# Kernel tuning notes

Measured on AMD Instinct MI355X. Metric: run time of the kernel, lower is better.

## Reference

```python
import jax, jax.numpy as jnp
import numpy as np

B, H, W, C = 4, 256, 256, 128
HEADS, WS, SHIFT = 4, 8, 4
EPS = 1e-5


def _rel_pos_index(ws):
    coords = np.stack(np.meshgrid(np.arange(ws), np.arange(ws), indexing='ij'))
    cf = coords.reshape(2, -1)
    rel = (cf[:, :, None] - cf[:, None, :]).transpose(1, 2, 0)
    rel[:, :, 0] += ws - 1
    rel[:, :, 1] += ws - 1
    rel[:, :, 0] *= 2 * ws - 1
    return rel.sum(-1).reshape(-1)

REL_IDX = jnp.array(_rel_pos_index(WS))


def _shift_mask(h, w, ws, shift):
    img = np.zeros((1, h, w, 1))
    cnt = 0
    sl = (slice(0, -ws), slice(-ws, -shift), slice(-shift, None))
    for hs in sl:
        for wsl in sl:
            img[:, hs, wsl, :] = cnt
            cnt += 1
    m = img.reshape(1, h // ws, ws, w // ws, ws, 1).transpose(0, 1, 3, 2, 4, 5).reshape(-1, ws * ws)
    am = m[:, None, :] - m[:, :, None]
    return jnp.array(np.where(am != 0, -100.0, 0.0).astype(np.float32))

ATTN_MASK = _shift_mask(H, W, WS, SHIFT)  # (nW, ws*ws, ws*ws)


def _ln(x, scale, bias):
    mu = x.mean(-1, keepdims=True)
    var = x.var(-1, keepdims=True)
    return (x - mu) / jnp.sqrt(var + EPS) * scale + bias


def setup_inputs() -> dict:
    key = jax.random.key(0)
    ks = jax.random.split(key, 8)
    s = 0.02
    return dict(
        hidden_states=jax.random.normal(ks[0], (B, H * W, C), jnp.float32),
        ln1_scale=jnp.ones((C,), jnp.float32), ln1_bias=jnp.zeros((C,), jnp.float32),
        q_w=jax.random.normal(ks[1], (C, C), jnp.float32) * s, q_b=jnp.zeros((C,), jnp.float32),
        k_w=jax.random.normal(ks[2], (C, C), jnp.float32) * s, k_b=jnp.zeros((C,), jnp.float32),
        v_w=jax.random.normal(ks[3], (C, C), jnp.float32) * s, v_b=jnp.zeros((C,), jnp.float32),
        proj_w=jax.random.normal(ks[4], (C, C), jnp.float32) * s, proj_b=jnp.zeros((C,), jnp.float32),
        rpb_table=jax.random.normal(ks[5], ((2 * WS - 1) ** 2, HEADS), jnp.float32) * s,
        ln2_scale=jnp.ones((C,), jnp.float32), ln2_bias=jnp.zeros((C,), jnp.float32),
        fc1_w=jax.random.normal(ks[6], (C, 4 * C), jnp.float32) * s, fc1_b=jnp.zeros((4 * C,), jnp.float32),
        fc2_w=jax.random.normal(ks[7], (4 * C, C), jnp.float32) * s, fc2_b=jnp.zeros((C,), jnp.float32),
    )


def reference(hidden_states, ln1_scale, ln1_bias, q_w, q_b, k_w, k_b, v_w, v_b,
              proj_w, proj_b, rpb_table, ln2_scale, ln2_bias, fc1_w, fc1_b, fc2_w, fc2_b):
    hd = C // HEADS
    T = WS * WS
    nW = (H // WS) * (W // WS)
    shortcut = hidden_states
    x = _ln(hidden_states, ln1_scale, ln1_bias).reshape(B, H, W, C)
    # cyclic shift
    x = jnp.roll(x, (-SHIFT, -SHIFT), axis=(1, 2))
    # window partition -> (B*nW, T, C)
    x = x.reshape(B, H // WS, WS, W // WS, WS, C).transpose(0, 1, 3, 2, 4, 5).reshape(-1, T, C)
    q = (x @ q_w + q_b).reshape(-1, T, HEADS, hd) / jnp.sqrt(jnp.float32(hd))
    k = (x @ k_w + k_b).reshape(-1, T, HEADS, hd)
    v = (x @ v_w + v_b).reshape(-1, T, HEADS, hd)
    attn = jnp.einsum('bqhd,bkhd->bhqk', q, k)
    bias = rpb_table[REL_IDX].reshape(T, T, HEADS).transpose(2, 0, 1)  # (h, q, k)
    attn = attn + bias[None]
    # shift mask per window
    attn = attn.reshape(B, nW, HEADS, T, T) + ATTN_MASK[None, :, None]
    attn = jax.nn.softmax(attn.reshape(-1, HEADS, T, T), axis=-1)
    out = jnp.einsum('bhqk,bkhd->bqhd', attn, v).reshape(-1, T, C)
    out = out @ proj_w + proj_b
    # window reverse + un-shift
    out = out.reshape(B, H // WS, W // WS, WS, WS, C).transpose(0, 1, 3, 2, 4, 5).reshape(B, H, W, C)
    out = jnp.roll(out, (SHIFT, SHIFT), axis=(1, 2)).reshape(B, H * W, C)
    x = shortcut + out
    y = _ln(x, ln2_scale, ln2_bias)
    y = jax.nn.gelu(y @ fc1_w + fc1_b, approximate=False) @ fc2_w + fc2_b
    return x + y
```

## Files before the change

### kernel.cpp

```cpp
#include <hip/hip_runtime.h>
#include <hip/hip_bf16.h>
#include <math.h>

#define B_ 4
#define H_ 256
#define W_ 256
#define C_ 128
#define HEADS_ 4
#define HD_ 32
#define WS_ 8
#define SHIFT_ 4
#define T_ 64
#define NW_ 1024
#define M_ (B_*NW_*T_)

typedef float floatx4 __attribute__((ext_vector_type(4)));
typedef short bf16x8 __attribute__((ext_vector_type(8)));
typedef unsigned short ushort8v __attribute__((ext_vector_type(8)));

#define MFMA16(a,b,c) __builtin_amdgcn_mfma_f32_16x16x32_bf16(a,b,c,0,0,0)

__device__ __forceinline__ unsigned short f2b(float f){
    union { float f; unsigned int i; } c; c.f = f;
    unsigned int r = c.i + 0x7FFFu + ((c.i >> 16) & 1u);
    return (unsigned short)(r >> 16);
}
__device__ __forceinline__ int region_id(int x){ return (x < 248) ? 0 : ((x < 252) ? 1 : 2); }

__device__ __forceinline__ bf16x8 ldfrag(const unsigned short* p){
    return *(const bf16x8*)p;
}
__device__ __forceinline__ bf16x8 ldfrag_strided(const unsigned short* p, int stride){
    ushort8v u;
    #pragma unroll
    for (int j = 0; j < 8; j++) u[j] = p[j*stride];
    return __builtin_bit_cast(bf16x8, u);
}
__device__ __forceinline__ floatx4 fzero(){ floatx4 v = {0.f,0.f,0.f,0.f}; return v; }

__device__ __forceinline__ float gelu_fast(float x){
    float z = x * 0.70710678118654752f;
    float az = fabsf(z);
    float t = __builtin_amdgcn_rcpf(fmaf(0.3275911f, az, 1.0f));
    float poly = t*(0.254829592f + t*(-0.284496736f + t*(1.421413741f +
                 t*(-1.453152027f + t*1.061405429f))));
    float e = __expf(-z*z);
    float er = 1.0f - poly*e;
    er = (z < 0.f) ? -er : er;
    return 0.5f * x * (1.0f + er);
}

#define WSO_QT   0
#define WSO_KT   16384
#define WSO_VT   32768
#define WSO_PT   49152
#define WSO_W1T  65536
#define WSO_W2T  131072
#define WSO_BIAS 196608
#define WS_BYTES_NEEDED (196608u*2u + 16384u*4u)

__global__ __launch_bounds__(256) void prep_weights_kernel(
        const float* __restrict__ qw, const float* __restrict__ kw,
        const float* __restrict__ vw, const float* __restrict__ pw,
        const float* __restrict__ fc1, const float* __restrict__ fc2,
        const float* __restrict__ rpb, unsigned short* __restrict__ ws)
{
    int tid = blockIdx.x * 256 + threadIdx.x;
    int nt = gridDim.x * 256;
    for (int i = tid; i < 16384; i += nt) {
        int n = i >> 7, k = i & 127;
        ws[WSO_QT + i] = f2b(qw[k*128 + n]);
        ws[WSO_KT + i] = f2b(kw[k*128 + n]);
        ws[WSO_VT + i] = f2b(vw[k*128 + n]);
        ws[WSO_PT + i] = f2b(pw[k*128 + n]);
    }
    for (int i = tid; i < 65536; i += nt) {
        int n = i >> 7, k = i & 127;
        ws[WSO_W1T + i] = f2b(fc1[(size_t)k*512 + n]);
    }
    for (int i = tid; i < 65536; i += nt) {
        int n = i >> 9, k = i & 511;
        ws[WSO_W2T + i] = f2b(fc2[(size_t)k*128 + n]);
    }
    float* bt = (float*)(ws + WSO_BIAS);
    for (int i = tid; i < 16384; i += nt) {
        int h = i >> 12, q = (i >> 6) & 63, k = i & 63;
        int th = q >> 3, tw = q & 7, jh = k >> 3, jw = k & 7;
        bt[i] = rpb[((th - jh + 7)*15 + (tw - jw + 7))*HEADS_ + h];
    }
}

__device__ __forceinline__ void gemm64x128_g(
        const unsigned short (*Xs)[136], const unsigned short* __restrict__ Wt,
        int wv, int quad, int l15, floatx4 acc[4][2])
{
    #pragma unroll
    for (int c = 0; c < 4; c++) {
        bf16x8 bf0 = ldfrag(Wt + (size_t)(32*wv + l15)*128      + c*32 + quad*8);
        bf16x8 bf1 = ldfrag(Wt + (size_t)(32*wv + 16 + l15)*128 + c*32 + quad*8);
        #pragma unroll
        for (int m = 0; m < 4; m++) {
            bf16x8 af = ldfrag(&Xs[16*m + l15][c*32 + quad*8]);
            acc[m][0] = MFMA16(af, bf0, acc[m][0]);
            acc[m][1] = MFMA16(af, bf1, acc[m][1]);
        }
    }
}

__global__ __launch_bounds__(256) void swin_attn_kernel4(
        const float* __restrict__ hidden,
        const float* __restrict__ ln1_s, const float* __restrict__ ln1_b,
        const float* __restrict__ q_b, const float* __restrict__ k_b,
        const float* __restrict__ v_b, const float* __restrict__ p_b,
        const unsigned short* __restrict__ wsu,
        float* __restrict__ xres)
{
    __shared__ __align__(16) unsigned short SH[2][T_][136];
    __shared__ __align__(16) unsigned short Vs[T_][134];
    __shared__ __align__(16) unsigned short PhD[4][2560];
    unsigned short (*Xs)[136] = SH[0];
    unsigned short (*Ks)[136] = SH[1];

    int tid = threadIdx.x;
    int wv = tid >> 6, lane = tid & 63;
    int quad = lane >> 4, l15 = lane & 15;
    int gw = blockIdx.x;
    int wi = gw & (NW_-1), b = gw >> 10;
    int hb = wi >> 5, wb = wi & 31;

    {
        int rloc = lane >> 2;
        int t = wv*16 + rloc;
        int th = t >> 3, tw = t & 7;
        int h = (hb*8 + th + SHIFT_) & 255;
        int w = (wb*8 + tw + SHIFT_) & 255;
        int c0 = (lane & 3) * 32;
        const float* xp = hidden + ((size_t)((b<<16) + (h<<8) + w)) * C_ + c0;
        float4 xv[8];
        float s = 0.f, ss = 0.f;
        #pragma unroll
        for (int i = 0; i < 8; i++) {
            xv[i] = *((const float4*)xp + i);
            s  += xv[i].x + xv[i].y + xv[i].z + xv[i].w;
            ss += xv[i].x*xv[i].x + xv[i].y*xv[i].y + xv[i].z*xv[i].z + xv[i].w*xv[i].w;
        }
        s  += __shfl_xor(s, 1, 64);  s  += __shfl_xor(s, 2, 64);
        ss += __shfl_xor(ss, 1, 64); ss += __shfl_xor(ss, 2, 64);
        float mean = s * (1.0f/C_);
        float var  = ss * (1.0f/C_) - mean*mean;
        float rstd = __builtin_amdgcn_rsqf(var + 1e-5f);
        #pragma unroll
        for (int i = 0; i < 8; i++) {
            float4 sc = *((const float4*)(ln1_s + c0) + i);
            float4 bi = *((const float4*)(ln1_b + c0) + i);
            ushort4 o;
            o.x = f2b((xv[i].x - mean)*rstd*sc.x + bi.x);
            o.y = f2b((xv[i].y - mean)*rstd*sc.y + bi.y);
            o.z = f2b((xv[i].z - mean)*rstd*sc.z + bi.z);
            o.w = f2b((xv[i].w - mean)*rstd*sc.w + bi.w);
            *(ushort4*)&Xs[t][c0 + 4*i] = o;
        }
    }
    __syncthreads();

    floatx4 qacc[4][2];
    {
        floatx4 kacc[4][2], vacc[4][2];
        #pragma unroll
        for (int m = 0; m < 4; m++) {
            qacc[m][0] = fzero(); qacc[m][1] = fzero();
            kacc[m][0] = fzero(); kacc[m][1] = fzero();
            vacc[m][0] = fzero(); vacc[m][1] = fzero();
        }
        const unsigned short* Qt = wsu + WSO_QT;
        const unsigned short* Kt = wsu + WSO_KT;
        const unsigned short* Vt = wsu + WSO_VT;
        #pragma unroll
        for (int c = 0; c < 4; c++) {
            size_t off0 = (size_t)(32*wv + l15)*128      + c*32 + quad*8;
            size_t off1 = (size_t)(32*wv + 16 + l15)*128 + c*32 + quad*8;
            bf16x8 qf0 = ldfrag(Qt + off0), qf1 = ldfrag(Qt + off1);
            bf16x8 kf0 = ldfrag(Kt + off0), kf1 = ldfrag(Kt + off1);
            bf16x8 vf0 = ldfrag(Vt + off0), vf1 = ldfrag(Vt + off1);
            #pragma unroll
            for (int m = 0; m < 4; m++) {
                bf16x8 af = ldfrag(&Xs[16*m + l15][c*32 + quad*8]);
                qacc[m][0] = MFMA16(af, qf0, qacc[m][0]);
                qacc[m][1] = MFMA16(af, qf1, qacc[m][1]);
                kacc[m][0] = MFMA16(af, kf0, kacc[m][0]);
                kacc[m][1] = MFMA16(af, kf1, kacc[m][1]);
                vacc[m][0] = MFMA16(af, vf0, vacc[m][0]);
                vacc[m][1] = MFMA16(af, vf1, vacc[m][1]);
            }
        }
        float kb0 = k_b[32*wv + l15], kb1 = k_b[32*wv + 16 + l15];
        float vb0 = v_b[32*wv + l15], vb1 = v_b[32*wv + 16 + l15];
        #pragma unroll
        for (int m = 0; m < 4; m++)
            #pragma unroll
            for (int r = 0; r < 4; r++) {
                int q = 16*m + 4*quad + r;
                Ks[q][32*wv + l15]      = f2b(kacc[m][0][r] + kb0);
                Ks[q][32*wv + 16 + l15] = f2b(kacc[m][1][r] + kb1);
                Vs[q][32*wv + l15]      = f2b(vacc[m][0][r] + vb0);
                Vs[q][32*wv + 16 + l15] = f2b(vacc[m][1][r] + vb1);
            }
    }
    __syncthreads();
    {
        const float sc = 0.17677669529663687f;
        float qb0 = q_b[32*wv + l15], qb1 = q_b[32*wv + 16 + l15];
        #pragma unroll
        for (int m = 0; m < 4; m++)
            #pragma unroll
            for (int r = 0; r < 4; r++) {
                int q = 16*m + 4*quad + r;
                Xs[q][32*wv + l15]      = f2b((qacc[m][0][r] + qb0) * sc);
                Xs[q][32*wv + 16 + l15] = f2b((qacc[m][1][r] + qb1) * sc);
            }
    }

    floatx4 sacc[4][4];
    #pragma unroll
    for (int m = 0; m < 4; m++)
        #pragma unroll
        for (int n = 0; n < 4; n++) sacc[m][n] = fzero();
    {
        bf16x8 qf[4], kf[4];
        #pragma unroll
        for (int m = 0; m < 4; m++) qf[m] = ldfrag(&Xs[16*m + l15][32*wv + quad*8]);
        #pragma unroll
        for (int n = 0; n < 4; n++) kf[n] = ldfrag(&Ks[16*n + l15][32*wv + quad*8]);
        #pragma unroll
        for (int m = 0; m < 4; m++)
            #pragma unroll
            for (int n = 0; n < 4; n++) sacc[m][n] = MFMA16(kf[n], qf[m], sacc[m][n]);
    }

    {
        const float* bt = (const float*)(wsu + WSO_BIAS) + (wv << 12);
        int cidk[4][4];
        #pragma unroll
        for (int n = 0; n < 4; n++)
            #pragma unroll
            for (int r = 0; r < 4; r++) {
                int kt = 16*n + 4*quad + r;
                cidk[n][r] = region_id(hb*8 + (kt >> 3))*3 + region_id(wb*8 + (kt & 7));
            }
        #pragma unroll
        for (int m = 0; m < 4; m++) {
            int q = 16*m + l15;
            int cidq = region_id(hb*8 + (q >> 3))*3 + region_id(wb*8 + (q & 7));
            float v[4][4];
            float mx = -3.0e38f;
            #pragma unroll
            for (int n = 0; n < 4; n++) {
                float4 bv = *(const float4*)(bt + q*64 + 16*n + 4*quad);
                #pragma unroll
                for (int r = 0; r < 4; r++) {
                    float d = sacc[m][n][r] + bv[r];
                    if (cidq != cidk[n][r]) d -= 100.f;
                    v[n][r] = d;
                    mx = fmaxf(mx, d);
                }
            }
            mx = fmaxf(mx, __shfl_xor(mx, 16, 64));
            mx = fmaxf(mx, __shfl_xor(mx, 32, 64));
            float sum = 0.f;
            #pragma unroll
            for (int n = 0; n < 4; n++)
                #pragma unroll
                for (int r = 0; r < 4; r++) { v[n][r] = __expf(v[n][r] - mx); sum += v[n][r]; }
            sum += __shfl_xor(sum, 16, 64);
            sum += __shfl_xor(sum, 32, 64);
            float inv = __builtin_amdgcn_rcpf(sum);
            #pragma unroll
            for (int n = 0; n < 4; n++)
                #pragma unroll
                for (int r = 0; r < 4; r++) sacc[m][n][r] = v[n][r] * inv;
        }
    }

    unsigned short* Ph = PhD[wv];
    floatx4 oacc[4][2];
    #pragma unroll
    for (int m = 0; m < 4; m++) { oacc[m][0] = fzero(); oacc[m][1] = fzero(); }
    #pragma unroll
    for (int kb = 0; kb < 2; kb++) {
        #pragma unroll
        for (int m = 0; m < 4; m++)
            #pragma unroll
            for (int n2 = 0; n2 < 2; n2++)
                #pragma unroll
                for (int r = 0; r < 4; r++)
                    Ph[(16*m + l15)*40 + n2*16 + 4*quad + r] = f2b(sacc[m][2*kb + n2][r]);
        bf16x8 bf0 = ldfrag_strided(&Vs[kb*32 + quad*8][32*wv + l15],      134);
        bf16x8 bf1 = ldfrag_strided(&Vs[kb*32 + quad*8][32*wv + 16 + l15], 134);
        #pragma unroll
        for (int m = 0; m < 4; m++) {
            bf16x8 af = ldfrag(&Ph[(16*m + l15)*40 + quad*8]);
            oacc[m][0] = MFMA16(af, bf0, oacc[m][0]);
            oacc[m][1] = MFMA16(af, bf1, oacc[m][1]);
        }
    }
    #pragma unroll
    for (int m = 0; m < 4; m++)
        #pragma unroll
        for (int r = 0; r < 4; r++) {
            int q = 16*m + 4*quad + r;
            Xs[q][32*wv + l15]      = f2b(oacc[m][0][r]);
            Xs[q][32*wv + 16 + l15] = f2b(oacc[m][1][r]);
        }
    __syncthreads();
    floatx4 pacc[4][2];
    #pragma unroll
    for (int m = 0; m < 4; m++) { pacc[m][0] = fzero(); pacc[m][1] = fzero(); }
    gemm64x128_g(Xs, wsu + WSO_PT, wv, quad, l15, pacc);
    __syncthreads();
    {
        float* Fb = (float*)&SH[0][0][0];
        float pb0 = p_b[32*wv + l15], pb1 = p_b[32*wv + 16 + l15];
        #pragma unroll
        for (int m = 0; m < 4; m++)
            #pragma unroll
            for (int r = 0; r < 4; r++) {
                int q = 16*m + 4*quad + r;
                Fb[q*128 + 32*wv + l15]      = pacc[m][0][r] + pb0;
                Fb[q*128 + 32*wv + 16 + l15] = pacc[m][1][r] + pb1;
            }
        __syncthreads();
        int t = tid >> 2;
        int cs = (tid & 3) * 32;
        int th = t >> 3, tw = t & 7;
        int h = (hb*8 + th + SHIFT_) & 255;
        int w = (wb*8 + tw + SHIFT_) & 255;
        size_t dst = ((size_t)((b<<16) + (h<<8) + w)) * C_ + cs;
        const float4* hp = (const float4*)(hidden + dst);
        float4* op = (float4*)(xres + dst);
        const float4* fp = (const float4*)(Fb + t*128 + cs);
        #pragma unroll
        for (int i = 0; i < 8; i++) {
            float4 hv = hp[i];
            float4 fv = fp[i];
            float4 o; o.x = hv.x + fv.x; o.y = hv.y + fv.y;
            o.z = hv.z + fv.z; o.w = hv.w + fv.w;
            op[i] = o;
        }
    }
}

__global__ __launch_bounds__(256, 6) void mlp_ln_kernel4(
        float* __restrict__ xio,
        const float* __restrict__ ln2_s, const float* __restrict__ ln2_b,
        const float* __restrict__ b1, const float* __restrict__ b2,
        const unsigned short* __restrict__ wsu)
{
    __shared__ __align__(16) unsigned short As[T_][136];
    __shared__ __align__(16) unsigned short G[T_][72];
    const unsigned short* W1t = wsu + WSO_W1T;
    const unsigned short* W2t = wsu + WSO_W2T;
    int tid = threadIdx.x, wv = tid >> 6, lane = tid & 63;
    int quad = lane >> 4, l15 = lane & 15;
    size_t row0 = (size_t)blockIdx.x * 64;

    {
        int rloc = lane >> 2;
        int t = wv*16 + rloc;
        int c0 = (lane & 3) * 32;
        const float* xp = xio + (row0 + t)*C_ + c0;
        float4 xv[8];
        float s = 0.f, ss = 0.f;
        #pragma unroll
        for (int i = 0; i < 8; i++) {
            xv[i] = *((const float4*)xp + i);
            s  += xv[i].x + xv[i].y + xv[i].z + xv[i].w;
            ss += xv[i].x*xv[i].x + xv[i].y*xv[i].y + xv[i].z*xv[i].z + xv[i].w*xv[i].w;
        }
        s  += __shfl_xor(s, 1, 64);  s  += __shfl_xor(s, 2, 64);
        ss += __shfl_xor(ss, 1, 64); ss += __shfl_xor(ss, 2, 64);
        float mean = s * (1.0f/C_);
        float var  = ss * (1.0f/C_) - mean*mean;
        float rstd = __builtin_amdgcn_rsqf(var + 1e-5f);
        #pragma unroll
        for (int i = 0; i < 8; i++) {
            float4 sc = *((const float4*)(ln2_s + c0) + i);
            float4 bi = *((const float4*)(ln2_b + c0) + i);
            ushort4 o;
            o.x = f2b((xv[i].x - mean)*rstd*sc.x + bi.x);
            o.y = f2b((xv[i].y - mean)*rstd*sc.y + bi.y);
            o.z = f2b((xv[i].z - mean)*rstd*sc.z + bi.z);
            o.w = f2b((xv[i].w - mean)*rstd*sc.w + bi.w);
            *(ushort4*)&As[t][c0 + 4*i] = o;
        }
    }
    __syncthreads();

    floatx4 acc2[4][2];
    #pragma unroll
    for (int m = 0; m < 4; m++) { acc2[m][0] = fzero(); acc2[m][1] = fzero(); }

    for (int ch = 0; ch < 8; ch++) {
        floatx4 a1[4];
        #pragma unroll
        for (int m = 0; m < 4; m++) a1[m] = fzero();
        #pragma unroll
        for (int kc = 0; kc < 4; kc++) {
            bf16x8 bf = ldfrag(W1t + (size_t)(ch*64 + 16*wv + l15)*128 + kc*32 + quad*8);
            #pragma unroll
            for (int m = 0; m < 4; m++) {
                bf16x8 af = ldfrag(&As[16*m + l15][kc*32 + quad*8]);
                a1[m] = MFMA16(af, bf, a1[m]);
            }
        }
        __syncthreads();
        {
            int c_rel = 16*wv + l15;
            float bb = b1[ch*64 + c_rel];
            #pragma unroll
            for (int m = 0; m < 4; m++)
                #pragma unroll
                for (int r = 0; r < 4; r++) {
                    float hh = a1[m][r] + bb;
                    G[16*m + 4*quad + r][c_rel] = f2b(gelu_fast(hh));
                }
        }
        __syncthreads();
        #pragma unroll
        for (int ki = 0; ki < 2; ki++) {
            bf16x8 bf0 = ldfrag(W2t + (size_t)(32*wv + l15)*512      + ch*64 + ki*32 + quad*8);
            bf16x8 bf1 = ldfrag(W2t + (size_t)(32*wv + 16 + l15)*512 + ch*64 + ki*32 + quad*8);
            #pragma unroll
            for (int m = 0; m < 4; m++) {
                bf16x8 af = ldfrag(&G[16*m + l15][ki*32 + quad*8]);
                acc2[m][0] = MFMA16(af, bf0, acc2[m][0]);
                acc2[m][1] = MFMA16(af, bf1, acc2[m][1]);
            }
        }
    }
    {
        float bb0 = b2[32*wv + l15], bb1 = b2[32*wv + 16 + l15];
        #pragma unroll
        for (int m = 0; m < 4; m++)
            #pragma unroll
            for (int r = 0; r < 4; r++) {
                size_t rr = row0 + 16*m + 4*quad + r;
                int c0 = 32*wv + l15;
                xio[rr*C_ + c0]      += acc2[m][0][r] + bb0;
                xio[rr*C_ + c0 + 16] += acc2[m][1][r] + bb1;
            }
    }
}


__device__ __forceinline__ void gemm64x128(
        const unsigned short (*Xs)[136], unsigned short (*Wc)[132],
        const float* __restrict__ Wg, int tid, int wv, int quad, int l15,
        floatx4 acc[4][2])
{
    for (int c = 0; c < 4; c++) {
        __syncthreads();
        #pragma unroll
        for (int it = 0; it < 4; it++) {
            int idx = tid + it*256;
            int kk = idx >> 5;
            int n4 = (idx & 31) * 4;
            float4 v = *(const float4*)(Wg + (size_t)(c*32 + kk)*C_ + n4);
            ushort4 o; o.x=f2b(v.x); o.y=f2b(v.y); o.z=f2b(v.z); o.w=f2b(v.w);
            *(ushort4*)&Wc[kk][n4] = o;
        }
        __syncthreads();
        bf16x8 bf0 = ldfrag_strided(&Wc[quad*8][32*wv + l15],      132);
        bf16x8 bf1 = ldfrag_strided(&Wc[quad*8][32*wv + 16 + l15], 132);
        #pragma unroll
        for (int m = 0; m < 4; m++) {
            bf16x8 af = ldfrag(&Xs[16*m + l15][c*32 + quad*8]);
            acc[m][0] = MFMA16(af, bf0, acc[m][0]);
            acc[m][1] = MFMA16(af, bf1, acc[m][1]);
        }
    }
}

__global__ __launch_bounds__(256) void swin_attn_kernel(
        const float* __restrict__ hidden,
        const float* __restrict__ ln1_s, const float* __restrict__ ln1_b,
        const float* __restrict__ q_w, const float* __restrict__ q_b,
        const float* __restrict__ k_w, const float* __restrict__ k_b,
        const float* __restrict__ v_w, const float* __restrict__ v_b,
        const float* __restrict__ p_w, const float* __restrict__ p_b,
        const float* __restrict__ rpb,
        float* __restrict__ xres)
{
    __shared__ unsigned short Xs[T_][136];
    __shared__ unsigned short Ks[T_][136];
    __shared__ unsigned short Vs[T_][134];
    __shared__ __align__(16) unsigned char U[10240];

    unsigned short (*Wc)[132] = (unsigned short(*)[132])U;
    float* rpbf = (float*)U;

    int tid = threadIdx.x;
    int wv = tid >> 6, lane = tid & 63;
    int quad = lane >> 4, l15 = lane & 15;
    int gw = blockIdx.x;
    int wi = gw & (NW_-1), b = gw >> 10;
    int hb = wi >> 5, wb = wi & 31;

    for (int it = 0; it < 16; it++) {
        int t = wv*16 + it;
        int th = t >> 3, tw = t & 7;
        int h = (hb*8 + th + SHIFT_) & 255;
        int w = (wb*8 + tw + SHIFT_) & 255;
        size_t src = ((size_t)((b<<16) + (h<<8) + w)) * C_;
        float2 u = *(const float2*)(hidden + src + 2*lane);
        float x0 = u.x, x1 = u.y;
        float s = x0 + x1, ss = x0*x0 + x1*x1;
        #pragma unroll
        for (int m = 32; m > 0; m >>= 1) {
            s  += __shfl_xor(s,  m, 64);
            ss += __shfl_xor(ss, m, 64);
        }
        float mean = s * (1.0f/C_);
        float var  = ss * (1.0f/C_) - mean*mean;
        float rstd = rsqrtf(var + 1e-5f);
        int c0 = 2*lane;
        ushort2 o;
        o.x = f2b((x0 - mean) * rstd * ln1_s[c0]   + ln1_b[c0]);
        o.y = f2b((x1 - mean) * rstd * ln1_s[c0+1] + ln1_b[c0+1]);
        *(ushort2*)&Xs[t][c0] = o;
    }

    {
        floatx4 acc[4][2];
        #pragma unroll
        for (int m = 0; m < 4; m++) { acc[m][0] = fzero(); acc[m][1] = fzero(); }
        gemm64x128(Xs, Wc, k_w, tid, wv, quad, l15, acc);
        float kb0 = k_b[32*wv + l15], kb1 = k_b[32*wv + 16 + l15];
        #pragma unroll
        for (int m = 0; m < 4; m++)
            #pragma unroll
            for (int r = 0; r < 4; r++) {
                int q = 16*m + 4*quad + r;
                Ks[q][32*wv + l15]      = f2b(acc[m][0][r] + kb0);
                Ks[q][32*wv + 16 + l15] = f2b(acc[m][1][r] + kb1);
            }
    }
    {
        floatx4 acc[4][2];
        #pragma unroll
        for (int m = 0; m < 4; m++) { acc[m][0] = fzero(); acc[m][1] = fzero(); }
        gemm64x128(Xs, Wc, v_w, tid, wv, quad, l15, acc);
        float vb0 = v_b[32*wv + l15], vb1 = v_b[32*wv + 16 + l15];
        #pragma unroll
        for (int m = 0; m < 4; m++)
            #pragma unroll
            for (int r = 0; r < 4; r++) {
                int q = 16*m + 4*quad + r;
                Vs[q][32*wv + l15]      = f2b(acc[m][0][r] + vb0);
                Vs[q][32*wv + 16 + l15] = f2b(acc[m][1][r] + vb1);
            }
    }
    floatx4 qacc[4][2];
    #pragma unroll
    for (int m = 0; m < 4; m++) { qacc[m][0] = fzero(); qacc[m][1] = fzero(); }
    gemm64x128(Xs, Wc, q_w, tid, wv, quad, l15, qacc);
    __syncthreads();
    for (int i = tid; i < 225*HEADS_; i += 256) rpbf[i] = rpb[i];
    {
        const float sc = 0.17677669529663687f;
        float qb0 = q_b[32*wv + l15], qb1 = q_b[32*wv + 16 + l15];
        #pragma unroll
        for (int m = 0; m < 4; m++)
            #pragma unroll
            for (int r = 0; r < 4; r++) {
                int q = 16*m + 4*quad + r;
                Xs[q][32*wv + l15]      = f2b((qacc[m][0][r] + qb0) * sc);
                Xs[q][32*wv + 16 + l15] = f2b((qacc[m][1][r] + qb1) * sc);
            }
    }
    __syncthreads();

    floatx4 sacc[4][4];
    #pragma unroll
    for (int m = 0; m < 4; m++)
        #pragma unroll
        for (int n = 0; n < 4; n++) sacc[m][n] = fzero();
    {
        bf16x8 qf[4], kf[4];
        #pragma unroll
        for (int m = 0; m < 4; m++) qf[m] = ldfrag(&Xs[16*m + l15][32*wv + quad*8]);
        #pragma unroll
        for (int n = 0; n < 4; n++) kf[n] = ldfrag(&Ks[16*n + l15][32*wv + quad*8]);
        #pragma unroll
        for (int m = 0; m < 4; m++)
            #pragma unroll
            for (int n = 0; n < 4; n++) sacc[m][n] = MFMA16(qf[m], kf[n], sacc[m][n]);
    }
    {
        int jh_[4], jw_[4], cidj_[4];
        #pragma unroll
        for (int n = 0; n < 4; n++) {
            int kt = 16*n + l15;
            jh_[n] = kt >> 3; jw_[n] = kt & 7;
            cidj_[n] = region_id(hb*8 + jh_[n])*3 + region_id(wb*8 + jw_[n]);
        }
        #pragma unroll
        for (int m = 0; m < 4; m++)
            #pragma unroll
            for (int r = 0; r < 4; r++) {
                int q = 16*m + 4*quad + r;
                int th = q >> 3, twq = q & 7;
                int cidi = region_id(hb*8 + th)*3 + region_id(wb*8 + twq);
                float v[4];
                #pragma unroll
                for (int n = 0; n < 4; n++) {
                    float d = sacc[m][n][r];
                    d += rpbf[((th - jh_[n] + 7)*15 + (twq - jw_[n] + 7))*HEADS_ + wv];
                    if (cidi != cidj_[n]) d -= 100.f;
                    v[n] = d;
                }
                float mx = fmaxf(fmaxf(v[0],v[1]), fmaxf(v[2],v[3]));
                #pragma unroll
                for (int off = 1; off < 16; off <<= 1) mx = fmaxf(mx, __shfl_xor(mx, off, 64));
                float sum = 0.f;
                #pragma unroll
                for (int n = 0; n < 4; n++) { v[n] = __expf(v[n] - mx); sum += v[n]; }
                #pragma unroll
                for (int off = 1; off < 16; off <<= 1) sum += __shfl_xor(sum, off, 64);
                float inv = 1.0f / sum;
                #pragma unroll
                for (int n = 0; n < 4; n++) sacc[m][n][r] = v[n] * inv;
            }
    }
    __syncthreads();

    unsigned short* Ph = (wv < 2) ? (&Ks[0][0] + wv*2560)
                                  : ((unsigned short*)U + (wv-2)*2560);
    floatx4 oacc[4][2];
    #pragma unroll
    for (int m = 0; m < 4; m++) { oacc[m][0] = fzero(); oacc[m][1] = fzero(); }
    for (int kb = 0; kb < 2; kb++) {
        #pragma unroll
        for (int m = 0; m < 4; m++)
            #pragma unroll
            for (int r = 0; r < 4; r++) {
                int q = 16*m + 4*quad + r;
                Ph[q*40 + l15]      = f2b(sacc[m][2*kb+0][r]);
                Ph[q*40 + 16 + l15] = f2b(sacc[m][2*kb+1][r]);
            }
        __syncthreads();
        bf16x8 bf0 = ldfrag_strided(&Vs[kb*32 + quad*8][32*wv + l15],      134);
        bf16x8 bf1 = ldfrag_strided(&Vs[kb*32 + quad*8][32*wv + 16 + l15], 134);
        #pragma unroll
        for (int m = 0; m < 4; m++) {
            bf16x8 af = ldfrag(&Ph[(16*m + l15)*40 + quad*8]);
            oacc[m][0] = MFMA16(af, bf0, oacc[m][0]);
            oacc[m][1] = MFMA16(af, bf1, oacc[m][1]);
        }
        __syncthreads();
    }
    #pragma unroll
    for (int m = 0; m < 4; m++)
        #pragma unroll
        for (int r = 0; r < 4; r++) {
            int q = 16*m + 4*quad + r;
            Xs[q][32*wv + l15]      = f2b(oacc[m][0][r]);
            Xs[q][32*wv + 16 + l15] = f2b(oacc[m][1][r]);
        }
    {
        floatx4 acc[4][2];
        #pragma unroll
        for (int m = 0; m < 4; m++) { acc[m][0] = fzero(); acc[m][1] = fzero(); }
        gemm64x128(Xs, Wc, p_w, tid, wv, quad, l15, acc);
        float pb0 = p_b[32*wv + l15], pb1 = p_b[32*wv + 16 + l15];
        #pragma unroll
        for (int m = 0; m < 4; m++)
            #pragma unroll
            for (int r = 0; r < 4; r++) {
                int t = 16*m + 4*quad + r;
                int th = t >> 3, tw = t & 7;
                int h = (hb*8 + th + SHIFT_) & 255;
                int w = (wb*8 + tw + SHIFT_) & 255;
                size_t dst = ((size_t)((b<<16) + (h<<8) + w)) * C_;
                int c0 = 32*wv + l15;
                xres[dst + c0]      = hidden[dst + c0]      + acc[m][0][r] + pb0;
                xres[dst + c0 + 16] = hidden[dst + c0 + 16] + acc[m][1][r] + pb1;
            }
    }
}

__global__ __launch_bounds__(256) void mlp_ln_kernel(
        float* __restrict__ xio,
        const float* __restrict__ ln2_s, const float* __restrict__ ln2_b,
        const float* __restrict__ W1, const float* __restrict__ b1,
        const float* __restrict__ W2, const float* __restrict__ b2)
{
    __shared__ unsigned short As[T_][136];
    __shared__ unsigned short G[T_][72];
    __shared__ unsigned short W1c[C_][68];
    __shared__ unsigned short W2c[T_][132];
    int tid = threadIdx.x, wv = tid >> 6, lane = tid & 63;
    int quad = lane >> 4, l15 = lane & 15;
    size_t row0 = (size_t)blockIdx.x * 64;

    for (int it = 0; it < 16; it++) {
        int t = wv*16 + it;
        const float* xp = xio + (row0 + t)*C_;
        float2 u = *(const float2*)(xp + 2*lane);
        float x0 = u.x, x1 = u.y;
        float s = x0 + x1, ss = x0*x0 + x1*x1;
        #pragma unroll
        for (int m = 32; m > 0; m >>= 1) {
            s  += __shfl_xor(s,  m, 64);
            ss += __shfl_xor(ss, m, 64);
        }
        float mean = s * (1.0f/C_);
        float var  = ss * (1.0f/C_) - mean*mean;
        float rstd = rsqrtf(var + 1e-5f);
        int c0 = 2*lane;
        ushort2 o;
        o.x = f2b((x0 - mean) * rstd * ln2_s[c0]   + ln2_b[c0]);
        o.y = f2b((x1 - mean) * rstd * ln2_s[c0+1] + ln2_b[c0+1]);
        *(ushort2*)&As[t][c0] = o;
    }

    floatx4 acc2[4][2];
    #pragma unroll
    for (int m = 0; m < 4; m++) { acc2[m][0] = fzero(); acc2[m][1] = fzero(); }

    for (int ch = 0; ch < 8; ch++) {
        __syncthreads();
        #pragma unroll
        for (int it = 0; it < 8; it++) {
            int idx = tid + it*256;
            int k = idx >> 4, n4 = (idx & 15) * 4;
            float4 v = *(const float4*)(W1 + (size_t)k*512 + ch*64 + n4);
            ushort4 o; o.x=f2b(v.x); o.y=f2b(v.y); o.z=f2b(v.z); o.w=f2b(v.w);
            *(ushort4*)&W1c[k][n4] = o;
        }
        #pragma unroll
        for (int it = 0; it < 8; it++) {
            int idx = tid + it*256;
            int k = idx >> 5, n4 = (idx & 31) * 4;
            float4 v = *(const float4*)(W2 + (size_t)(ch*64 + k)*C_ + n4);
            ushort4 o; o.x=f2b(v.x); o.y=f2b(v.y); o.z=f2b(v.z); o.w=f2b(v.w);
            *(ushort4*)&W2c[k][n4] = o;
        }
        __syncthreads();
        floatx4 a1[4];
        #pragma unroll
        for (int m = 0; m < 4; m++) a1[m] = fzero();
        #pragma unroll
        for (int kc = 0; kc < 4; kc++) {
            bf16x8 bfrag = ldfrag_strided(&W1c[kc*32 + quad*8][16*wv + l15], 68);
            #pragma unroll
            for (int m = 0; m < 4; m++) {
                bf16x8 af = ldfrag(&As[16*m + l15][kc*32 + quad*8]);
                a1[m] = MFMA16(af, bfrag, a1[m]);
            }
        }
        {
            int c_rel = 16*wv + l15;
            float bb = b1[ch*64 + c_rel];
            #pragma unroll
            for (int m = 0; m < 4; m++)
                #pragma unroll
                for (int r = 0; r < 4; r++) {
                    int q = 16*m + 4*quad + r;
                    float hh = a1[m][r] + bb;
                    float g = 0.5f * hh * (1.0f + erff(hh * 0.70710678118654752f));
                    G[q][c_rel] = f2b(g);
                }
        }
        __syncthreads();
        #pragma unroll
        for (int ki = 0; ki < 2; ki++) {
            bf16x8 bf0 = ldfrag_strided(&W2c[ki*32 + quad*8][32*wv + l15],      132);
            bf16x8 bf1 = ldfrag_strided(&W2c[ki*32 + quad*8][32*wv + 16 + l15], 132);
            #pragma unroll
            for (int m = 0; m < 4; m++) {
                bf16x8 af = ldfrag(&G[16*m + l15][ki*32 + quad*8]);
                acc2[m][0] = MFMA16(af, bf0, acc2[m][0]);
                acc2[m][1] = MFMA16(af, bf1, acc2[m][1]);
            }
        }
    }
    {
        float bb0 = b2[32*wv + l15], bb1 = b2[32*wv + 16 + l15];
        #pragma unroll
        for (int m = 0; m < 4; m++)
            #pragma unroll
            for (int r = 0; r < 4; r++) {
                size_t rr = row0 + 16*m + 4*quad + r;
                int c0 = 32*wv + l15;
                xio[rr*C_ + c0]      += acc2[m][0][r] + bb0;
                xio[rr*C_ + c0 + 16] += acc2[m][1][r] + bb1;
            }
    }
}

extern "C" void kernel_launch(void* const* d_in, const int* in_sizes, int n_in,
                              void* d_out, int out_size, void* d_ws, size_t ws_size,
                              hipStream_t stream) {
    (void)in_sizes; (void)n_in; (void)out_size;
    const float* hidden = (const float*)d_in[0];
    const float* ln1_s  = (const float*)d_in[1];
    const float* ln1_b  = (const float*)d_in[2];
    const float* q_w    = (const float*)d_in[3];
    const float* q_b    = (const float*)d_in[4];
    const float* k_w    = (const float*)d_in[5];
    const float* k_b    = (const float*)d_in[6];
    const float* v_w    = (const float*)d_in[7];
    const float* v_b    = (const float*)d_in[8];
    const float* p_w    = (const float*)d_in[9];
    const float* p_b    = (const float*)d_in[10];
    const float* rpb    = (const float*)d_in[11];
    const float* ln2_s  = (const float*)d_in[12];
    const float* ln2_b  = (const float*)d_in[13];
    const float* fc1_w  = (const float*)d_in[14];
    const float* fc1_b  = (const float*)d_in[15];
    const float* fc2_w  = (const float*)d_in[16];
    const float* fc2_b  = (const float*)d_in[17];
    float* outp = (float*)d_out;

    if (d_ws != nullptr && ws_size >= (size_t)WS_BYTES_NEEDED) {
        unsigned short* wsu = (unsigned short*)d_ws;
        prep_weights_kernel<<<64, 256, 0, stream>>>(q_w, k_w, v_w, p_w,
                fc1_w, fc2_w, rpb, wsu);
        swin_attn_kernel4<<<B_*NW_, 256, 0, stream>>>(hidden, ln1_s, ln1_b,
                q_b, k_b, v_b, p_b, wsu, outp);
        mlp_ln_kernel4<<<M_/64, 256, 0, stream>>>(outp, ln2_s, ln2_b,
                fc1_b, fc2_b, wsu);
    } else {
        swin_attn_kernel<<<B_*NW_, 256, 0, stream>>>(hidden, ln1_s, ln1_b,
                q_w, q_b, k_w, k_b, v_w, v_b, p_w, p_b, rpb, outp);
        mlp_ln_kernel<<<M_/64, 256, 0, stream>>>(outp, ln2_s, ln2_b,
                fc1_w, fc1_b, fc2_w, fc2_b);
    }
}
```

Measured before the change: 577.1 us.

## Fuse window attention and MLP into one kernel with shared LDS reuse

```diff
diff --git a/kernel.cpp b/kernel.cpp
--- a/kernel.cpp
+++ b/kernel.cpp
@@ -107,17 +107,18 @@
     }
 }
 
-__global__ __launch_bounds__(256) void swin_attn_kernel4(
+__global__ __launch_bounds__(256, 3) void swin_fused_kernel(
         const float* __restrict__ hidden,
         const float* __restrict__ ln1_s, const float* __restrict__ ln1_b,
         const float* __restrict__ q_b, const float* __restrict__ k_b,
         const float* __restrict__ v_b, const float* __restrict__ p_b,
+        const float* __restrict__ ln2_s, const float* __restrict__ ln2_b,
+        const float* __restrict__ b1, const float* __restrict__ b2,
         const unsigned short* __restrict__ wsu,
-        float* __restrict__ xres)
+        float* __restrict__ outp)
 {
     __shared__ __align__(16) unsigned short SH[2][T_][136];
-    __shared__ __align__(16) unsigned short Vs[T_][134];
-    __shared__ __align__(16) unsigned short PhD[4][2560];
+    __shared__ __align__(16) unsigned short VsT[C_][72];
     unsigned short (*Xs)[136] = SH[0];
     unsigned short (*Ks)[136] = SH[1];
 
@@ -202,8 +203,8 @@
                 int q = 16*m + 4*quad + r;
                 Ks[q][32*wv + l15]      = f2b(kacc[m][0][r] + kb0);
                 Ks[q][32*wv + 16 + l15] = f2b(kacc[m][1][r] + kb1);
-                Vs[q][32*wv + l15]      = f2b(vacc[m][0][r] + vb0);
-                Vs[q][32*wv + 16 + l15] = f2b(vacc[m][1][r] + vb1);
+                VsT[32*wv + l15][q]      = f2b(vacc[m][0][r] + vb0);
+                VsT[32*wv + 16 + l15][q] = f2b(vacc[m][1][r] + vb1);
             }
     }
     __syncthreads();
@@ -280,8 +281,9 @@
                 for (int r = 0; r < 4; r++) sacc[m][n][r] = v[n][r] * inv;
         }
     }
-
-    unsigned short* Ph = PhD[wv];
+    __syncthreads();
+
+    unsigned short* Ph = (wv < 2) ? (&Ks[0][0] + wv*2560) : (&Xs[0][0] + (wv-2)*2560);
     floatx4 oacc[4][2];
     #pragma unroll
     for (int m = 0; m < 4; m++) { oacc[m][0] = fzero(); oacc[m][1] = fzero(); }
@@ -294,8 +296,8 @@
                 #pragma unroll
                 for (int r = 0; r < 4; r++)
                     Ph[(16*m + l15)*40 + n2*16 + 4*quad + r] = f2b(sacc[m][2*kb + n2][r]);
-        bf16x8 bf0 = ldfrag_strided(&Vs[kb*32 + quad*8][32*wv + l15],      134);
-        bf16x8 bf1 = ldfrag_strided(&Vs[kb*32 + quad*8][32*wv + 16 + l15], 134);
+        bf16x8 bf0 = ldfrag(&VsT[32*wv + l15][kb*32 + quad*8]);
+        bf16x8 bf1 = ldfrag(&VsT[32*wv + 16 + l15][kb*32 + quad*8]);
         #pragma unroll
         for (int m = 0; m < 4; m++) {
             bf16x8 af = ldfrag(&Ph[(16*m + l15)*40 + quad*8]);
@@ -303,6 +305,7 @@
             oacc[m][1] = MFMA16(af, bf1, oacc[m][1]);
         }
     }
+    __syncthreads();
     #pragma unroll
     for (int m = 0; m < 4; m++)
         #pragma unroll
@@ -312,62 +315,45 @@
             Xs[q][32*wv + 16 + l15] = f2b(oacc[m][1][r]);
         }
     __syncthreads();
+
     floatx4 pacc[4][2];
     #pragma unroll
     for (int m = 0; m < 4; m++) { pacc[m][0] = fzero(); pacc[m][1] = fzero(); }
     gemm64x128_g(Xs, wsu + WSO_PT, wv, quad, l15, pacc);
-    __syncthreads();
-    {
-        float* Fb = (float*)&SH[0][0][0];
+    {
         float pb0 = p_b[32*wv + l15], pb1 = p_b[32*wv + 16 + l15];
         #pragma unroll
         for (int m = 0; m < 4; m++)
             #pragma unroll
             for (int r = 0; r < 4; r++) {
-                int q = 16*m + 4*quad + r;
-                Fb[q*128 + 32*wv + l15]      = pacc[m][0][r] + pb0;
-                Fb[q*128 + 32*wv + 16 + l15] = pacc[m][1][r] + pb1;
-            }
-        __syncthreads();
-        int t = tid >> 2;
-        int cs = (tid & 3) * 32;
-        int th = t >> 3, tw = t & 7;
-        int h = (hb*8 + th + SHIFT_) & 255;
-        int w = (wb*8 + tw + SHIFT_) & 255;
-        size_t dst = ((size_t)((b<<16) + (h<<8) + w)) * C_ + cs;
-        const float4* hp = (const float4*)(hidden + dst);
-        float4* op = (float4*)(xres + dst);
-        const float4* fp = (const float4*)(Fb + t*128 + cs);
-        #pragma unroll
-        for (int i = 0; i < 8; i++) {
-            float4 hv = hp[i];
-            float4 fv = fp[i];
-            float4 o; o.x = hv.x + fv.x; o.y = hv.y + fv.y;
-            o.z = hv.z + fv.z; o.w = hv.w + fv.w;
-            op[i] = o;
-        }
-    }
-}
-
-__global__ __launch_bounds__(256, 6) void mlp_ln_kernel4(
-        float* __restrict__ xio,
-        const float* __restrict__ ln2_s, const float* __restrict__ ln2_b,
-        const float* __restrict__ b1, const float* __restrict__ b2,
-        const unsigned short* __restrict__ wsu)
-{
-    __shared__ __align__(16) unsigned short As[T_][136];
-    __shared__ __align__(16) unsigned short G[T_][72];
-    const unsigned short* W1t = wsu + WSO_W1T;
-    const unsigned short* W2t = wsu + WSO_W2T;
-    int tid = threadIdx.x, wv = tid >> 6, lane = tid & 63;
-    int quad = lane >> 4, l15 = lane & 15;
-    size_t row0 = (size_t)blockIdx.x * 64;
-
+                int t = 16*m + 4*quad + r;
+                int th = t >> 3, tw = t & 7;
+                int h = (hb*8 + th + SHIFT_) & 255;
+                int w = (wb*8 + tw + SHIFT_) & 255;
+                size_t src = ((size_t)((b<<16) + (h<<8) + w)) * C_;
+                pacc[m][0][r] += pb0 + hidden[src + 32*wv + l15];
+                pacc[m][1][r] += pb1 + hidden[src + 32*wv + 16 + l15];
+            }
+    }
+    __syncthreads();
+
+    float* Fb = (float*)&SH[0][0][0];
+    #pragma unroll
+    for (int m = 0; m < 4; m++)
+        #pragma unroll
+        for (int r = 0; r < 4; r++) {
+            int q = 16*m + 4*quad + r;
+            Fb[q*132 + 32*wv + l15]      = pacc[m][0][r];
+            Fb[q*132 + 32*wv + 16 + l15] = pacc[m][1][r];
+        }
+    __syncthreads();
+
+    unsigned short (*As)[136] = (unsigned short(*)[136])&VsT[0][0];
     {
         int rloc = lane >> 2;
         int t = wv*16 + rloc;
         int c0 = (lane & 3) * 32;
-        const float* xp = xio + (row0 + t)*C_ + c0;
+        const float* xp = Fb + t*132 + c0;
         float4 xv[8];
         float s = 0.f, ss = 0.f;
         #pragma unroll
@@ -395,6 +381,9 @@
     }
     __syncthreads();
 
+    unsigned short (*G)[72] = (unsigned short(*)[72])&SH[0][0][0];
+    const unsigned short* W1t = wsu + WSO_W1T;
+    const unsigned short* W2t = wsu + WSO_W2T;
     floatx4 acc2[4][2];
     #pragma unroll
     for (int m = 0; m < 4; m++) { acc2[m][0] = fzero(); acc2[m][1] = fzero(); }
@@ -437,17 +426,29 @@
             }
         }
     }
+    __syncthreads();
+
     {
         float bb0 = b2[32*wv + l15], bb1 = b2[32*wv + 16 + l15];
         #pragma unroll
         for (int m = 0; m < 4; m++)
             #pragma unroll
             for (int r = 0; r < 4; r++) {
-                size_t rr = row0 + 16*m + 4*quad + r;
-                int c0 = 32*wv + l15;
-                xio[rr*C_ + c0]      += acc2[m][0][r] + bb0;
-                xio[rr*C_ + c0 + 16] += acc2[m][1][r] + bb1;
-            }
+                int q = 16*m + 4*quad + r;
+                Fb[q*132 + 32*wv + l15]      = pacc[m][0][r] + acc2[m][0][r] + bb0;
+                Fb[q*132 + 32*wv + 16 + l15] = pacc[m][1][r] + acc2[m][1][r] + bb1;
+            }
+        __syncthreads();
+        int t = tid >> 2;
+        int cs = (tid & 3) * 32;
+        int th = t >> 3, tw = t & 7;
+        int h = (hb*8 + th + SHIFT_) & 255;
+        int w = (wb*8 + tw + SHIFT_) & 255;
+        size_t dst = ((size_t)((b<<16) + (h<<8) + w)) * C_ + cs;
+        float4* op = (float4*)(outp + dst);
+        const float4* fp = (const float4*)(Fb + t*132 + cs);
+        #pragma unroll
+        for (int i = 0; i < 8; i++) op[i] = fp[i];
     }
 }
 
@@ -826,10 +827,8 @@
         unsigned short* wsu = (unsigned short*)d_ws;
         prep_weights_kernel<<<64, 256, 0, stream>>>(q_w, k_w, v_w, p_w,
                 fc1_w, fc2_w, rpb, wsu);
-        swin_attn_kernel4<<<B_*NW_, 256, 0, stream>>>(hidden, ln1_s, ln1_b,
-                q_b, k_b, v_b, p_b, wsu, outp);
-        mlp_ln_kernel4<<<M_/64, 256, 0, stream>>>(outp, ln2_s, ln2_b,
-                fc1_b, fc2_b, wsu);
+        swin_fused_kernel<<<B_*NW_, 256, 0, stream>>>(hidden, ln1_s, ln1_b,
+                q_b, k_b, v_b, p_b, ln2_s, ln2_b, fc1_b, fc2_b, wsu, outp);
     } else {
         swin_attn_kernel<<<B_*NW_, 256, 0, stream>>>(hidden, ln1_s, ln1_b,
                 q_w, q_b, k_w, k_b, v_w, v_b, p_w, p_b, rpb, outp);
```

Result: no change. 568.2 us (-1.5%).
